# Performance work log

Hardware: AMD Instinct MI355X
Metric: run time of the kernel (lower is better)

Reference implementation:

```python
import jax, jax.numpy as jnp
import numpy as np

DIM = 1024
NUM_HEADS = 16
HEAD_DIM = 64
INNER = NUM_HEADS * HEAD_DIM  # 1024
SCALE = HEAD_DIM ** -0.5


def setup_inputs() -> dict:
    key = jax.random.key(0)
    k1, k2, k3, k4 = jax.random.split(key, 4)
    x = jax.random.normal(k1, (4, 2048, DIM), dtype=jnp.float32)
    # Linear weights stored as [in, out] for x @ W
    w_qkv = jax.random.normal(k2, (DIM, INNER * 3), dtype=jnp.float32) * (DIM ** -0.5)
    w_out = jax.random.normal(k3, (INNER, DIM), dtype=jnp.float32) * (INNER ** -0.5)
    b_out = jax.random.normal(k4, (DIM,), dtype=jnp.float32) * 0.02
    return {"x": x, "w_qkv": w_qkv, "w_out": w_out, "b_out": b_out}


def reference(x, w_qkv, w_out, b_out):
    b, n, _ = x.shape
    qkv = x @ w_qkv  # [b, n, 3*inner]
    q, k, v = jnp.split(qkv, 3, axis=-1)
    # [b, n, inner] -> [b, h, n, d]
    split_heads = lambda t: t.reshape(b, n, NUM_HEADS, HEAD_DIM).transpose(0, 2, 1, 3)
    q, k, v = split_heads(q), split_heads(k), split_heads(v)
    scores = jnp.einsum('bhid,bhjd->bhij', q, k) * SCALE  # [b, h, n, n]
    weights = jax.nn.softmax(scores, axis=-1)
    attended = jnp.einsum('bhij,bhjd->bhid', weights, v)  # [b, h, n, d]
    attended = attended.transpose(0, 2, 1, 3).reshape(b, n, INNER)
    return attended @ w_out + b_out
```

## Files before the change

kernel.cpp:

```cpp
#include <hip/hip_runtime.h>
#include <hip/hip_bf16.h>

typedef __attribute__((ext_vector_type(8))) short short8;
typedef __attribute__((ext_vector_type(4))) short short4v;
typedef __attribute__((ext_vector_type(4))) float f32x4;

#define DIM    1024
#define NHEADS 16
#define HDIM   64
#define SEQ    2048
#define BATCH  4
#define ROWS   8192
#define QKV_N  3072

#define QSCALE_LOG2E 0.18033688011112042f

__device__ __forceinline__ unsigned short f2bf(float f) {
    union { float f; unsigned u; } v; v.f = f;
    unsigned u = v.u;
    return (unsigned short)((u + 0x7fffu + ((u >> 16) & 1u)) >> 16);
}
__device__ __forceinline__ float exp2_fast(float x) {
    float r;
    asm("v_exp_f32 %0, %1" : "=v"(r) : "v"(x));
    return r;
}
__device__ __forceinline__ unsigned cvt_pk_bf16(float a, float b) {
    unsigned r;
    asm("v_cvt_pk_bf16_f32 %0, %1, %2" : "=v"(r) : "v"(a), "v"(b));
    return r;
}

__device__ __forceinline__ void gload16(const void* g, void* l) {
    __builtin_amdgcn_global_load_lds(
        (const __attribute__((address_space(1))) unsigned int*)g,
        (__attribute__((address_space(3))) unsigned int*)l, 16, 0, 0);
}

#define MFMA16(a, b, c) __builtin_amdgcn_mfma_f32_16x16x32_bf16(a, b, c, 0, 0, 0)

__global__ __launch_bounds__(256)
void conv_kernel(const float* __restrict__ src, unsigned short* __restrict__ dst, int n4)
{
    const int i = blockIdx.x * 256 + threadIdx.x;
    if (i >= n4) return;
    const float4 v = ((const float4*)src)[i];
    short4v o;
    o[0] = (short)f2bf(v.x); o[1] = (short)f2bf(v.y);
    o[2] = (short)f2bf(v.z); o[3] = (short)f2bf(v.w);
    ((short4v*)dst)[i] = o;
}

__global__ __launch_bounds__(256)
void convT_kernel(const float* __restrict__ src, unsigned short* __restrict__ dst,
                  int R, int C)
{
    __shared__ float T[32][33];
    const int r0 = blockIdx.y * 32, c0 = blockIdx.x * 32;
    const int tc = threadIdx.x & 31, tr = threadIdx.x >> 5;
    #pragma unroll
    for (int i = 0; i < 4; ++i)
        T[tr + i * 8][tc] = src[(size_t)(r0 + tr + i * 8) * C + c0 + tc];
    __syncthreads();
    #pragma unroll
    for (int i = 0; i < 4; ++i)
        dst[(size_t)(c0 + tr + i * 8) * R + r0 + tc] = f2bf(T[tc][tr + i * 8]);
}

template<bool WITH_BIAS, bool QSCALE>
__global__ __launch_bounds__(256)
void gemm_kernel(const unsigned short* __restrict__ A,
                 const unsigned short* __restrict__ BT,
                 const float* __restrict__ bias,
                 void* __restrict__ Cp, int M, int N, int K)
{
    __shared__ alignas(16) unsigned short LA[128][32];
    __shared__ alignas(16) unsigned short LB[128][32];

    const int tid  = threadIdx.x;
    const int lane = tid & 63;
    const int w    = tid >> 6;
    const int wr   = w >> 1, wc = w & 1;
    const int bm   = blockIdx.y * 128, bn = blockIdx.x * 128;
    const int r16  = lane & 15, g = lane >> 4;

    f32x4 acc[4][4] = {};

    const int srow = lane >> 2, skg = (lane & 3) * 8;

    for (int k0 = 0; k0 < K; k0 += 32) {
        #pragma unroll
        for (int c = 0; c < 2; ++c) {
            const int chunk = w * 2 + c;
            gload16(A  + (size_t)(bm + chunk * 16 + srow) * K + k0 + skg, &LA[chunk * 16][0]);
            gload16(BT + (size_t)(bn + chunk * 16 + srow) * K + k0 + skg, &LB[chunk * 16][0]);
        }
        __syncthreads();
        short8 af[4], bf_[4];
        #pragma unroll
        for (int i = 0; i < 4; ++i) {
            af[i]  = *(const short8*)&LA[wr * 64 + i * 16 + r16][g * 8];
            bf_[i] = *(const short8*)&LB[wc * 64 + i * 16 + r16][g * 8];
        }
        __builtin_amdgcn_s_setprio(1);
        #pragma unroll
        for (int mi = 0; mi < 4; ++mi)
            #pragma unroll
            for (int ni = 0; ni < 4; ++ni)
                acc[mi][ni] = MFMA16(af[mi], bf_[ni], acc[mi][ni]);
        __builtin_amdgcn_s_setprio(0);
        __syncthreads();
    }

    #pragma unroll
    for (int mi = 0; mi < 4; ++mi)
        #pragma unroll
        for (int ni = 0; ni < 4; ++ni) {
            const int gcol = bn + wc * 64 + ni * 16 + r16;
            #pragma unroll
            for (int j = 0; j < 4; ++j) {
                const int grow = bm + wr * 64 + mi * 16 + g * 4 + j;
                float v = acc[mi][ni][j];
                if (QSCALE && gcol < DIM) v *= QSCALE_LOG2E;
                if (WITH_BIAS)
                    ((float*)Cp)[(size_t)grow * N + gcol] = v + bias[gcol];
                else
                    ((unsigned short*)Cp)[(size_t)grow * N + gcol] = f2bf(v);
            }
        }
}

__global__ __launch_bounds__(256, 4)
void attn_kernel(const unsigned short* __restrict__ qkv,
                 unsigned short* __restrict__ att)
{
    __shared__ alignas(16) unsigned short Ks[2][64][64];
    __shared__ alignas(16) unsigned short Vt[80][80];

    const int tid  = threadIdx.x;
    const int lane = tid & 63;
    const int w    = tid >> 6;
    const int b  = blockIdx.z, h = blockIdx.y;
    const int q0 = blockIdx.x * 128;
    const size_t base = (size_t)b * SEQ * QKV_N + (size_t)h * HDIM;

    const int r16 = lane & 15;
    const int g   = lane >> 4;
    const int f7  = r16 & 7;

    if (tid < 80) Vt[64][tid] = 0x3F80;
    for (int idx = tid; idx < 15 * 80; idx += 256)
        Vt[65 + idx / 80][idx % 80] = 0;
    __syncthreads();

    const int krow  = lane >> 3;
    const int kGsrc = (lane & 7) ^ (krow & 7);

    #pragma unroll
    for (int c = 0; c < 2; ++c) {
        const int chunk = w * 2 + c;
        gload16(qkv + base + (size_t)(chunk * 8 + krow) * QKV_N + DIM + kGsrc * 8,
                &Ks[0][chunk * 8][0]);
    }

    short8 qf[2][2];
    #pragma unroll
    for (int mi = 0; mi < 2; ++mi) {
        const unsigned short* qrow =
            qkv + base + (size_t)(q0 + w * 32 + mi * 16 + r16) * QKV_N;
        qf[mi][0] = *(const short8*)(qrow + g * 8);
        qf[mi][1] = *(const short8*)(qrow + 32 + g * 8);
    }

    f32x4 oacc[2][5] = {};
    float m_r[2] = { -3e38f, -3e38f };

    const int k5 = lane & 31, khi = lane >> 5;
    const int vpos = ((k5 < 16) ? ((k5 >> 2) * 8 + (k5 & 3))
                                : (((k5 - 16) >> 2) * 8 + 4 + ((k5 - 16) & 3)))
                     + khi * 32;

    for (int kt = 0; kt < SEQ; kt += 64) {
        const int buf = (kt >> 6) & 1;

        const unsigned short* vsrc =
            qkv + base + (size_t)(kt + lane) * QKV_N + 2 * DIM + w * 16;
        short8 v0 = *(const short8*)(vsrc);
        short8 v1 = *(const short8*)(vsrc + 8);

        if (kt + 64 < SEQ) {
            #pragma unroll
            for (int c = 0; c < 2; ++c) {
                const int chunk = w * 2 + c;
                gload16(qkv + base + (size_t)(kt + 64 + chunk * 8 + krow) * QKV_N
                        + DIM + kGsrc * 8,
                        &Ks[buf ^ 1][chunk * 8][0]);
            }
            asm volatile("s_waitcnt vmcnt(4)" ::: "memory");
        } else {
            asm volatile("s_waitcnt vmcnt(2)" ::: "memory");
        }
        __builtin_amdgcn_s_barrier();
        __builtin_amdgcn_sched_barrier(0);

        f32x4 sacc[2][4] = {};
        __builtin_amdgcn_s_setprio(1);
        #pragma unroll
        for (int jt = 0; jt < 4; ++jt) {
            const int row = jt * 16 + r16;
            short8 kf0 = *(const short8*)&Ks[buf][row][(g ^ f7) * 8];
            short8 kf1 = *(const short8*)&Ks[buf][row][((4 + g) ^ f7) * 8];
            sacc[0][jt] = MFMA16(kf0, qf[0][0], sacc[0][jt]);
            sacc[0][jt] = MFMA16(kf1, qf[0][1], sacc[0][jt]);
            sacc[1][jt] = MFMA16(kf0, qf[1][0], sacc[1][jt]);
            sacc[1][jt] = MFMA16(kf1, qf[1][1], sacc[1][jt]);
        }
        __builtin_amdgcn_s_setprio(0);

        short8 pb[2][2];
        #pragma unroll
        for (int mi = 0; mi < 2; ++mi) {
            const float a0 = fmaxf(fmaxf(sacc[mi][0][0], sacc[mi][0][1]), sacc[mi][0][2]);
            const float a1 = fmaxf(fmaxf(sacc[mi][0][3], sacc[mi][1][0]), sacc[mi][1][1]);
            const float a2 = fmaxf(fmaxf(sacc[mi][1][2], sacc[mi][1][3]), sacc[mi][2][0]);
            const float a3 = fmaxf(fmaxf(sacc[mi][2][1], sacc[mi][2][2]), sacc[mi][2][3]);
            const float a4 = fmaxf(fmaxf(sacc[mi][3][0], sacc[mi][3][1]), sacc[mi][3][2]);
            float tm = fmaxf(fmaxf(fmaxf(a0, a1), a2),
                             fmaxf(fmaxf(a3, a4), sacc[mi][3][3]));
            tm = fmaxf(tm, __shfl_xor(tm, 16));
            tm = fmaxf(tm, __shfl_xor(tm, 32));

            float nm = m_r[mi];
            if (!__all(tm <= m_r[mi] + 8.f)) {
                nm = fmaxf(m_r[mi], tm);
                const float f = exp2_fast(m_r[mi] - nm);
                m_r[mi] = nm;
                #pragma unroll
                for (int dt = 0; dt < 5; ++dt)
                    #pragma unroll
                    for (int jr = 0; jr < 4; ++jr)
                        oacc[mi][dt][jr] *= f;
            }

            unsigned pw[8];
            #pragma unroll
            for (int jt = 0; jt < 4; ++jt) {
                const float p0 = exp2_fast(sacc[mi][jt][0] - nm);
                const float p1 = exp2_fast(sacc[mi][jt][1] - nm);
                const float p2 = exp2_fast(sacc[mi][jt][2] - nm);
                const float p3 = exp2_fast(sacc[mi][jt][3] - nm);
                pw[jt * 2]     = cvt_pk_bf16(p0, p1);
                pw[jt * 2 + 1] = cvt_pk_bf16(p2, p3);
            }

            union { unsigned u[4]; short8 s; } c0, c1;
            c0.u[0] = pw[0]; c0.u[1] = pw[1]; c0.u[2] = pw[2]; c0.u[3] = pw[3];
            c1.u[0] = pw[4]; c1.u[1] = pw[5]; c1.u[2] = pw[6]; c1.u[7 - 7] = c1.u[0];
            c1.u[0] = pw[4]; c1.u[1] = pw[5]; c1.u[2] = pw[6]; c1.u[3] = pw[7];
            pb[mi][0] = c0.s;
            pb[mi][1] = c1.s;
        }

        #pragma unroll
        for (int i = 0; i < 8; ++i) {
            Vt[w * 16 + i][vpos]     = (unsigned short)v0[i];
            Vt[w * 16 + 8 + i][vpos] = (unsigned short)v1[i];
        }
        asm volatile("s_waitcnt lgkmcnt(0)" ::: "memory");
        __builtin_amdgcn_s_barrier();
        __builtin_amdgcn_sched_barrier(0);

        __builtin_amdgcn_s_setprio(1);
        #pragma unroll
        for (int dt = 0; dt < 5; ++dt) {
            short8 vf0 = *(const short8*)&Vt[dt * 16 + r16][g * 8];
            short8 vf1 = *(const short8*)&Vt[dt * 16 + r16][32 + g * 8];
            #pragma unroll
            for (int mi = 0; mi < 2; ++mi) {
                oacc[mi][dt] = MFMA16(vf0, pb[mi][0], oacc[mi][dt]);
                oacc[mi][dt] = MFMA16(vf1, pb[mi][1], oacc[mi][dt]);
            }
        }
        __builtin_amdgcn_s_setprio(0);
    }

    #pragma unroll
    for (int mi = 0; mi < 2; ++mi) {
        const float inv = 1.f / __shfl(oacc[mi][4][0], r16);
        const int q = q0 + w * 32 + mi * 16 + r16;
        unsigned short* dst = att + (size_t)(b * SEQ + q) * DIM + h * HDIM;
        #pragma unroll
        for (int dt = 0; dt < 4; ++dt)
            #pragma unroll
            for (int jr = 0; jr < 4; ++jr)
                dst[dt * 16 + g * 4 + jr] = f2bf(oacc[mi][dt][jr] * inv);
    }
}

extern "C" void kernel_launch(void* const* d_in, const int* in_sizes, int n_in,
                              void* d_out, int out_size, void* d_ws, size_t ws_size,
                              hipStream_t stream)
{
    const float* x     = (const float*)d_in[0];
    const float* w_qkv = (const float*)d_in[1];
    const float* w_out = (const float*)d_in[2];
    const float* b_out = (const float*)d_in[3];
    float* out = (float*)d_out;

    unsigned short* qkv   = (unsigned short*)d_ws;
    unsigned short* xb    = qkv + 25165824;
    unsigned short* att   = xb;
    unsigned short* wqkvT = qkv + 33554432;
    unsigned short* woutT = qkv + 36700160;

    conv_kernel<<<dim3(ROWS * DIM / 4 / 256), 256, 0, stream>>>(x, xb, ROWS * DIM / 4);
    convT_kernel<<<dim3(QKV_N / 32, DIM / 32), 256, 0, stream>>>(w_qkv, wqkvT, DIM, QKV_N);
    convT_kernel<<<dim3(DIM / 32, DIM / 32), 256, 0, stream>>>(w_out, woutT, DIM, DIM);

    gemm_kernel<false, true><<<dim3(QKV_N / 128, ROWS / 128), 256, 0, stream>>>(
        xb, wqkvT, nullptr, qkv, ROWS, QKV_N, DIM);

    attn_kernel<<<dim3(SEQ / 128, NHEADS, BATCH), 256, 0, stream>>>(qkv, att);

    gemm_kernel<true, false><<<dim3(DIM / 128, ROWS / 128), 256, 0, stream>>>(
        att, woutT, b_out, out, ROWS, DIM, DIM);
}
```

Measured before the change: 212.6 us.

## Double-buffer transposed V tile to drop second per-iteration barrier

Moves the V global load and its transposed LDS write one tile ahead into a double-buffered Vd array, with the ones row for the softmax denominator kept in a separate Vones buffer. Each loop iteration now has one barrier instead of two, and V load latency overlaps the QK^T and softmax work. In exchange, the top-of-loop wait drains all memory counters (vmcnt(0)), which may expose K prefetch latency, and LDS use grows.

```diff
diff --git a/kernel.cpp b/kernel.cpp
--- a/kernel.cpp
+++ b/kernel.cpp
@@ -135,7 +135,8 @@
                  unsigned short* __restrict__ att)
 {
     __shared__ alignas(16) unsigned short Ks[2][64][64];
-    __shared__ alignas(16) unsigned short Vt[80][80];
+    __shared__ alignas(16) unsigned short Vd[2][64][80];
+    __shared__ alignas(16) unsigned short Vones[16][80];
 
     const int tid  = threadIdx.x;
     const int lane = tid & 63;
@@ -148,14 +149,24 @@
     const int g   = lane >> 4;
     const int f7  = r16 & 7;
 
-    if (tid < 80) Vt[64][tid] = 0x3F80;
-    for (int idx = tid; idx < 15 * 80; idx += 256)
-        Vt[65 + idx / 80][idx % 80] = 0;
-    __syncthreads();
+    for (int idx = tid; idx < 16 * 80; idx += 256)
+        Vones[idx / 80][idx % 80] = (idx < 80) ? 0x3F80 : 0;
 
     const int krow  = lane >> 3;
     const int kGsrc = (lane & 7) ^ (krow & 7);
 
+    const int k5 = lane & 31, khi = lane >> 5;
+    const int vpos = ((k5 < 16) ? ((k5 >> 2) * 8 + (k5 & 3))
+                                : (((k5 - 16) >> 2) * 8 + 4 + ((k5 - 16) & 3)))
+                     + khi * 32;
+
+    short8 pv0, pv1;
+    {
+        const unsigned short* vsrc =
+            qkv + base + (size_t)lane * QKV_N + 2 * DIM + w * 16;
+        pv0 = *(const short8*)(vsrc);
+        pv1 = *(const short8*)(vsrc + 8);
+    }
     #pragma unroll
     for (int c = 0; c < 2; ++c) {
         const int chunk = w * 2 + c;
@@ -172,23 +183,31 @@
         qf[mi][1] = *(const short8*)(qrow + 32 + g * 8);
     }
 
+    {
+        #pragma unroll
+        for (int i = 0; i < 8; ++i) {
+            Vd[0][w * 16 + i][vpos]     = (unsigned short)pv0[i];
+            Vd[0][w * 16 + 8 + i][vpos] = (unsigned short)pv1[i];
+        }
+    }
+
     f32x4 oacc[2][5] = {};
     float m_r[2] = { -3e38f, -3e38f };
 
-    const int k5 = lane & 31, khi = lane >> 5;
-    const int vpos = ((k5 < 16) ? ((k5 >> 2) * 8 + (k5 & 3))
-                                : (((k5 - 16) >> 2) * 8 + 4 + ((k5 - 16) & 3)))
-                     + khi * 32;
-
     for (int kt = 0; kt < SEQ; kt += 64) {
         const int buf = (kt >> 6) & 1;
-
-        const unsigned short* vsrc =
-            qkv + base + (size_t)(kt + lane) * QKV_N + 2 * DIM + w * 16;
-        short8 v0 = *(const short8*)(vsrc);
-        short8 v1 = *(const short8*)(vsrc + 8);
-
-        if (kt + 64 < SEQ) {
+        const bool pre = (kt + 64 < SEQ);
+
+        asm volatile("s_waitcnt vmcnt(0) lgkmcnt(0)" ::: "memory");
+        __builtin_amdgcn_s_barrier();
+        __builtin_amdgcn_sched_barrier(0);
+
+        short8 nv0, nv1;
+        if (pre) {
+            const unsigned short* vsrc =
+                qkv + base + (size_t)(kt + 64 + lane) * QKV_N + 2 * DIM + w * 16;
+            nv0 = *(const short8*)(vsrc);
+            nv1 = *(const short8*)(vsrc + 8);
             #pragma unroll
             for (int c = 0; c < 2; ++c) {
                 const int chunk = w * 2 + c;
@@ -196,12 +215,7 @@
                         + DIM + kGsrc * 8,
                         &Ks[buf ^ 1][chunk * 8][0]);
             }
-            asm volatile("s_waitcnt vmcnt(4)" ::: "memory");
-        } else {
-            asm volatile("s_waitcnt vmcnt(2)" ::: "memory");
-        }
-        __builtin_amdgcn_s_barrier();
-        __builtin_amdgcn_sched_barrier(0);
+        }
 
         f32x4 sacc[2][4] = {};
         __builtin_amdgcn_s_setprio(1);
@@ -255,30 +269,37 @@
 
             union { unsigned u[4]; short8 s; } c0, c1;
             c0.u[0] = pw[0]; c0.u[1] = pw[1]; c0.u[2] = pw[2]; c0.u[3] = pw[3];
-            c1.u[0] = pw[4]; c1.u[1] = pw[5]; c1.u[2] = pw[6]; c1.u[7 - 7] = c1.u[0];
             c1.u[0] = pw[4]; c1.u[1] = pw[5]; c1.u[2] = pw[6]; c1.u[3] = pw[7];
             pb[mi][0] = c0.s;
             pb[mi][1] = c1.s;
         }
 
-        #pragma unroll
-        for (int i = 0; i < 8; ++i) {
-            Vt[w * 16 + i][vpos]     = (unsigned short)v0[i];
-            Vt[w * 16 + 8 + i][vpos] = (unsigned short)v1[i];
-        }
-        asm volatile("s_waitcnt lgkmcnt(0)" ::: "memory");
-        __builtin_amdgcn_s_barrier();
-        __builtin_amdgcn_sched_barrier(0);
+        if (pre) {
+            #pragma unroll
+            for (int i = 0; i < 8; ++i) {
+                Vd[buf ^ 1][w * 16 + i][vpos]     = (unsigned short)nv0[i];
+                Vd[buf ^ 1][w * 16 + 8 + i][vpos] = (unsigned short)nv1[i];
+            }
+        }
 
         __builtin_amdgcn_s_setprio(1);
         #pragma unroll
-        for (int dt = 0; dt < 5; ++dt) {
-            short8 vf0 = *(const short8*)&Vt[dt * 16 + r16][g * 8];
-            short8 vf1 = *(const short8*)&Vt[dt * 16 + r16][32 + g * 8];
+        for (int dt = 0; dt < 4; ++dt) {
+            short8 vf0 = *(const short8*)&Vd[buf][dt * 16 + r16][g * 8];
+            short8 vf1 = *(const short8*)&Vd[buf][dt * 16 + r16][32 + g * 8];
             #pragma unroll
             for (int mi = 0; mi < 2; ++mi) {
                 oacc[mi][dt] = MFMA16(vf0, pb[mi][0], oacc[mi][dt]);
                 oacc[mi][dt] = MFMA16(vf1, pb[mi][1], oacc[mi][dt]);
+            }
+        }
+        {
+            short8 vf0 = *(const short8*)&Vones[r16][g * 8];
+            short8 vf1 = *(const short8*)&Vones[r16][32 + g * 8];
+            #pragma unroll
+            for (int mi = 0; mi < 2; ++mi) {
+                oacc[mi][4] = MFMA16(vf0, pb[mi][0], oacc[mi][4]);
+                oacc[mi][4] = MFMA16(vf1, pb[mi][1], oacc[mi][4]);
             }
         }
         __builtin_amdgcn_s_setprio(0);
```

Measured after the change: 210.9 us. Within noise of the previous version (-0.8%).
